# Kernel tuning notes

Measured on AMD Instinct MI355X. Metric: run time of the kernel, lower is better.

## Reference

```python
import jax, jax.numpy as jnp
import numpy as np

N, E, G = 50000, 800000, 64
NODE_DIM, HID, HEADS, EDGE_DIM = 128, 256, 4, 2
LAYER_IN = [NODE_DIM, HID, HID]
LAYER_HEADS = [HEADS, HEADS, 1]
BN_EPS = 1e-5


def setup_inputs() -> dict:
    key = jax.random.key(0)
    ks = iter(jax.random.split(key, 80))
    def nrm(shape, s=0.05):
        return jax.random.normal(next(ks), shape, jnp.float32) * s
    inp = {}
    inp['x'] = jax.random.normal(next(ks), (N, NODE_DIM), jnp.float32)
    inp['edge_index'] = jax.random.randint(next(ks), (2, E), 0, N, jnp.int32)
    inp['edge_attr'] = jax.random.normal(next(ks), (E, EDGE_DIM), jnp.float32)
    inp['batch'] = jnp.sort(jax.random.randint(next(ks), (N,), 0, G, jnp.int32))
    for i in range(3):
        H = LAYER_HEADS[i]; C = HID // H
        inp[f'W{i}'] = nrm((LAYER_IN[i], H * C))
        inp[f'asrc{i}'] = nrm((H, C))
        inp[f'adst{i}'] = nrm((H, C))
        inp[f'We{i}'] = nrm((EDGE_DIM, H * C))
        inp[f'aedge{i}'] = nrm((H, C))
        inp[f'bconv{i}'] = jnp.zeros((HID,), jnp.float32)
        inp[f'bn{i}_g'] = jnp.ones((HID,), jnp.float32)
        inp[f'bn{i}_b'] = jnp.zeros((HID,), jnp.float32)
        inp[f'bn{i}_m'] = nrm((HID,), 0.01)
        inp[f'bn{i}_v'] = jnp.ones((HID,), jnp.float32)
    inp['Wskip'] = nrm((NODE_DIM, HID))
    inp['bskip'] = jnp.zeros((HID,), jnp.float32)
    inp['Wp1'] = nrm((2 * HID, HID))
    inp['bp1'] = jnp.zeros((HID,), jnp.float32)
    inp['Wp2'] = nrm((HID, 1))
    inp['bp2'] = jnp.zeros((1,), jnp.float32)
    return inp


def gat_conv(x, src, dst, ea, W, a_s, a_d, We, a_e, b, H, concat):
    n = x.shape[0]
    C = W.shape[1] // H
    h = (x @ W).reshape(n, H, C)                      # [N,H,C]
    # attention logits per edge (src/dst node terms + edge term)
    al = ((h * a_s).sum(-1)[src]
          + (h * a_d).sum(-1)[dst]
          + ((ea @ We).reshape(-1, H, C) * a_e).sum(-1))  # [Et,H]
    al = jax.nn.leaky_relu(al, 0.2)
    # segment softmax over destination nodes
    amax = jax.ops.segment_max(al, dst, num_segments=n)
    ex = jnp.exp(al - amax[dst])
    den = jax.ops.segment_sum(ex, dst, num_segments=n)
    alpha = ex / (den[dst] + 1e-16)
    out = jax.ops.segment_sum(h[src] * alpha[..., None], dst, num_segments=n)  # [N,H,C]
    out = out.reshape(n, H * C) if concat else out.mean(axis=1)
    return out + b


def _forward(x, edge_index, edge_attr, batch, layer_params, Wskip, bskip, Wp1, bp1, Wp2, bp2):
    n = x.shape[0]
    # add self-loops (PyG GATConv default), edge_attr filled with mean
    loop = jnp.arange(n, dtype=edge_index.dtype)
    src = jnp.concatenate([edge_index[0], loop])
    dst = jnp.concatenate([edge_index[1], loop])
    ea = jnp.concatenate([edge_attr, jnp.broadcast_to(edge_attr.mean(0), (n, edge_attr.shape[1]))], axis=0)
    identity = x
    for i, (W, a_s, a_d, We, a_e, b, g, be, rm, rv) in enumerate(layer_params):
        layer_identity = (identity @ Wskip + bskip) if i == 0 else identity
        concat = i < 2
        H = LAYER_HEADS[i]
        h = gat_conv(x, src, dst, ea, W, a_s, a_d, We, a_e, b, H, concat)
        h = (h - rm) * jax.lax.rsqrt(rv + BN_EPS) * g + be   # BatchNorm1d (eval)
        h = jax.nn.elu(h)
        x = h + layer_identity
        identity = x
    # global mean + max pool per graph
    counts = jnp.maximum(jax.ops.segment_sum(jnp.ones((n,), x.dtype), batch, num_segments=G), 1.0)
    mean_pool = jax.ops.segment_sum(x, batch, num_segments=G) / counts[:, None]
    max_pool = jax.ops.segment_max(x, batch, num_segments=G)
    emb = jnp.concatenate([mean_pool, max_pool], axis=1)      # [G, 2*HID]
    hmid = jax.nn.relu(emb @ Wp1 + bp1)
    return hmid @ Wp2 + bp2                                   # [G, 1]


def reference(x, edge_index, edge_attr, batch,
              W0, asrc0, adst0, We0, aedge0, bconv0, bn0_g, bn0_b, bn0_m, bn0_v,
              W1, asrc1, adst1, We1, aedge1, bconv1, bn1_g, bn1_b, bn1_m, bn1_v,
              W2, asrc2, adst2, We2, aedge2, bconv2, bn2_g, bn2_b, bn2_m, bn2_v,
              Wskip, bskip, Wp1, bp1, Wp2, bp2):
    layer_params = [
        (W0, asrc0, adst0, We0, aedge0, bconv0, bn0_g, bn0_b, bn0_m, bn0_v),
        (W1, asrc1, adst1, We1, aedge1, bconv1, bn1_g, bn1_b, bn1_m, bn1_v),
        (W2, asrc2, adst2, We2, aedge2, bconv2, bn2_g, bn2_b, bn2_m, bn2_v),
    ]
    return _forward(x, edge_index, edge_attr, batch, layer_params, Wskip, bskip, Wp1, bp1, Wp2, bp2)
```

## Files before the change

kernel.cpp:

```cpp
#include <hip/hip_runtime.h>
#include <cfloat>

#define Nn 50000
#define Ee 800000
#define Etot (Ee + Nn)
#define Gg 64
#define HIDc 256
#define BN_EPS 1e-5f

typedef unsigned int   uint32;
typedef unsigned short ushort16;
typedef short  bf16x8 __attribute__((ext_vector_type(8)));
typedef float  f32x4  __attribute__((ext_vector_type(4)));

__device__ inline ushort16 f2bf(float f) {
    uint32 u = __float_as_uint(f);
    u = (u + 0x7fffu + ((u >> 16) & 1u)) >> 16;
    return (ushort16)u;
}
__device__ inline uint32 pack2(float a, float b) {
    return (uint32)f2bf(a) | ((uint32)f2bf(b) << 16);
}
__device__ inline uint32 fenc(float f) {
    uint32 b = __float_as_uint(f);
    return (b & 0x80000000u) ? ~b : (b | 0x80000000u);
}
__device__ inline float fdec(uint32 u) {
    uint32 b = (u & 0x80000000u) ? (u & 0x7fffffffu) : ~u;
    return __uint_as_float(b);
}

__device__ inline long ws_index(int c, int k, int KB) {
    int cb = c >> 4, m = c & 15, kb = k >> 5, q = (k >> 3) & 3, e = k & 7;
    return (((long)(cb * KB + kb) * 64 + q * 16 + m) << 3) + e;
}

#define CVT4 (Nn * 128 / 4)
#define CVT_BLKS ((CVT4 + 255) / 256)
#define EBKS ((Etot + 255) / 256)
__global__ __launch_bounds__(256) void prep_kernel(
        const float* __restrict__ ea, float* __restrict__ ea_s,
        const float* __restrict__ We0, const float* __restrict__ ae0,
        const float* __restrict__ We1, const float* __restrict__ ae1,
        const float* __restrict__ We2, const float* __restrict__ ae2,
        float* __restrict__ M,
        const float* __restrict__ W0, const float* __restrict__ Wskip,
        const float* __restrict__ W1, const float* __restrict__ W2,
        ushort16* __restrict__ WtC, ushort16* __restrict__ Wt1,
        ushort16* __restrict__ Wt2,
        const float* __restrict__ x, ushort16* __restrict__ xbf,
        const int* __restrict__ ei, int* __restrict__ counts) {
    int bid = blockIdx.x, t = threadIdx.x;
    if (bid < 256) {
        __shared__ float sh0[256], sh1[256];
        float s0 = 0.f, s1 = 0.f;
        for (int e = bid * 256 + t; e < Ee; e += 256 * 256) {
            s0 += ea[2 * e];
            s1 += ea[2 * e + 1];
        }
        sh0[t] = s0; sh1[t] = s1;
        __syncthreads();
        for (int off = 128; off > 0; off >>= 1) {
            if (t < off) { sh0[t] += sh0[t + off]; sh1[t] += sh1[t + off]; }
            __syncthreads();
        }
        if (t == 0) { atomicAdd(&ea_s[0], sh0[0]); atomicAdd(&ea_s[1], sh1[0]); }
    } else if (bid == 256) {
        if (t >= 18) return;
        int l = t < 8 ? 0 : (t < 16 ? 1 : 2);
        int r = t - l * 8;
        const float* We = (l == 0) ? We0 : (l == 1 ? We1 : We2);
        const float* ae = (l == 0) ? ae0 : (l == 1 ? ae1 : ae2);
        int Hl = (l < 2) ? 4 : 1;
        int Cl = 256 / Hl;
        int d = r / Hl, hh = r % Hl;
        float s = 0.f;
        for (int c = 0; c < Cl; ++c)
            s += We[d * 256 + hh * Cl + c] * ae[hh * Cl + c];
        M[l * 8 + r] = s;
    } else if (bid < 385) {
        int k = bid - 257;
        WtC[ws_index(t, k, 4)] = f2bf(W0[(long)k * 256 + t]);
    } else if (bid < 513) {
        int k = bid - 385;
        WtC[ws_index(256 + t, k, 4)] = f2bf(Wskip[(long)k * 256 + t]);
    } else if (bid < 769) {
        int k = bid - 513;
        Wt1[ws_index(t, k, 8)] = f2bf(W1[(long)k * 256 + t]);
    } else if (bid < 1025) {
        int k = bid - 769;
        Wt2[ws_index(t, k, 8)] = f2bf(W2[(long)k * 256 + t]);
    } else if (bid < 1025 + CVT_BLKS) {
        int i = (bid - 1025) * 256 + t;
        if (i < CVT4) {
            float4 v = *(const float4*)&x[i * 4];
            ushort4 o;
            o.x = f2bf(v.x); o.y = f2bf(v.y); o.z = f2bf(v.z); o.w = f2bf(v.w);
            *(ushort4*)&xbf[i * 4] = o;
        }
    } else {
        int e = (bid - 1025 - CVT_BLKS) * 256 + t;
        if (e < Etot) {
            int d = (e < Ee) ? ei[Ee + e] : (e - Ee);
            atomicAdd(&counts[d], 1);
        }
    }
}

__global__ void scan1_kernel(const int* __restrict__ in, int* __restrict__ inc,
                             int* __restrict__ bsums) {
    __shared__ int sh[256];
    int i = blockIdx.x * 256 + threadIdx.x;
    int v = (i < Nn) ? in[i] : 0;
    sh[threadIdx.x] = v;
    __syncthreads();
    for (int off = 1; off < 256; off <<= 1) {
        int t = ((int)threadIdx.x >= off) ? sh[threadIdx.x - off] : 0;
        __syncthreads();
        sh[threadIdx.x] += t;
        __syncthreads();
    }
    if (i < Nn) inc[i] = sh[threadIdx.x];
    if (threadIdx.x == 255) bsums[blockIdx.x] = sh[255];
}

__global__ void scan23_kernel(const int* __restrict__ inc, const int* __restrict__ bsums,
                              int* __restrict__ row_start, int* __restrict__ cursor, int nb) {
    __shared__ int sh[256];
    int b = blockIdx.x, t = threadIdx.x;
    sh[t] = (t < b && t < nb) ? bsums[t] : 0;
    __syncthreads();
    for (int off = 128; off > 0; off >>= 1) {
        if (t < off) sh[t] += sh[t + off];
        __syncthreads();
    }
    int base = sh[0];
    int i = b * 256 + t;
    if (i < Nn) {
        int v = inc[i] + base;
        row_start[i + 1] = v;
        cursor[i + 1] = v;
    }
    if (i == 0) { row_start[0] = 0; cursor[0] = 0; }
}

__global__ void scatter_kernel(const int* __restrict__ ei, const float* __restrict__ ea,
                               const float* __restrict__ ea_sum, int* __restrict__ cursor,
                               int* __restrict__ src_sorted, float* __restrict__ ea_sorted) {
    int e = blockIdx.x * blockDim.x + threadIdx.x;
    if (e >= Etot) return;
    int s, d; float e0, e1;
    if (e < Ee) {
        s = ei[e]; d = ei[Ee + e];
        e0 = ea[2 * e]; e1 = ea[2 * e + 1];
    } else {
        s = d = e - Ee;
        const float invE = 1.f / (float)Ee;
        e0 = ea_sum[0] * invE; e1 = ea_sum[1] * invE;
    }
    int pos = atomicAdd(&cursor[d], 1);
    src_sorted[pos] = s;
    ea_sorted[2 * pos]     = e0;
    ea_sorted[2 * pos + 1] = e1;
}

#define LDK 40
__global__ __launch_bounds__(256) void mfma_gemm_kernel(
        const ushort16* __restrict__ A,
        const ushort16* __restrict__ WS,
        uint32* __restrict__ outF,
        uint32* __restrict__ outS,
        const float* __restrict__ bskip,
        const float* __restrict__ a_s, const float* __restrict__ a_d,
        float* __restrict__ ssrc, float* __restrict__ sdst,
        int n, int K) {
    __shared__ ushort16 As[128 * LDK];
    const int t    = threadIdx.x;
    const int row0 = blockIdx.x * 128;
    const int c0   = blockIdx.y * 128;
    const bool isSkip = (outS != nullptr) && (c0 >= 256);
    const int cc0  = isSkip ? c0 - 256 : c0;
    const int wave = t >> 6, lane = t & 63;
    const int wr = wave >> 1, wc = wave & 1;
    const int l15 = lane & 15, quad = lane >> 4;
    const int KB = K >> 5;

    f32x4 acc[4][4];
#pragma unroll
    for (int j = 0; j < 4; ++j)
#pragma unroll
        for (int i = 0; i < 4; ++i) {
            acc[j][i][0] = 0.f; acc[j][i][1] = 0.f;
            acc[j][i][2] = 0.f; acc[j][i][3] = 0.f;
        }

    const int sm = t & 127;
    const int so = t >> 7;

    for (int k0 = 0; k0 < K; k0 += 32) {
        const int kb = k0 >> 5;
#pragma unroll
        for (int h = 0; h < 2; ++h) {
            int oct = so + 2 * h;
            int grow = row0 + sm;
            uint4 va = make_uint4(0, 0, 0, 0);
            if (grow < n) va = *(const uint4*)&A[(long)grow * K + k0 + 8 * oct];
            *(uint4*)&As[sm * LDK + 8 * oct] = va;
        }
        bf16x8 bfv[4];
#pragma unroll
        for (int j = 0; j < 4; ++j) {
            int cb = ((c0 + wc * 64) >> 4) + j;
            bfv[j] = *(const bf16x8*)&WS[(((long)cb * KB + kb) * 64 + lane) << 3];
        }
        __syncthreads();
        bf16x8 af[4];
#pragma unroll
        for (int i = 0; i < 4; ++i)
            af[i] = *(const bf16x8*)&As[(wr * 64 + i * 16 + l15) * LDK + quad * 8];
#pragma unroll
        for (int j = 0; j < 4; ++j)
#pragma unroll
            for (int i = 0; i < 4; ++i)
                acc[j][i] = __builtin_amdgcn_mfma_f32_16x16x32_bf16(
                    bfv[j], af[i], acc[j][i], 0, 0, 0);
        __syncthreads();
    }

    float4 bb[4];
#pragma unroll
    for (int j = 0; j < 4; ++j) {
        if (isSkip) bb[j] = *(const float4*)&bskip[cc0 + wc * 64 + j * 16 + quad * 4];
        else        bb[j] = make_float4(0.f, 0.f, 0.f, 0.f);
    }

    uint32* tgt = isSkip ? outS : outF;
#pragma unroll
    for (int i = 0; i < 4; ++i) {
        int row = row0 + wr * 64 + i * 16 + l15;
        if (row >= n) continue;
#pragma unroll
        for (int j = 0; j < 4; ++j) {
            int col = cc0 + wc * 64 + j * 16 + quad * 4;
            uint2 pk;
            pk.x = pack2(acc[j][i][0] + bb[j].x, acc[j][i][1] + bb[j].y);
            pk.y = pack2(acc[j][i][2] + bb[j].z, acc[j][i][3] + bb[j].w);
            *(uint2*)&tgt[(long)row * 128 + (col >> 1)] = pk;
        }
    }

    if (!isSkip && a_s != nullptr) {
        float4 asv[4], adv[4];
#pragma unroll
        for (int j = 0; j < 4; ++j) {
            int col = cc0 + wc * 64 + j * 16 + quad * 4;
            asv[j] = *(const float4*)&a_s[col];
            adv[j] = *(const float4*)&a_d[col];
        }
        const int part = (cc0 + wc * 64) >> 6;
#pragma unroll
        for (int i = 0; i < 4; ++i) {
            float ps = 0.f, pd = 0.f;
#pragma unroll
            for (int j = 0; j < 4; ++j) {
                ps += acc[j][i][0] * asv[j].x + acc[j][i][1] * asv[j].y
                    + acc[j][i][2] * asv[j].z + acc[j][i][3] * asv[j].w;
                pd += acc[j][i][0] * adv[j].x + acc[j][i][1] * adv[j].y
                    + acc[j][i][2] * adv[j].z + acc[j][i][3] * adv[j].w;
            }
            ps += __shfl_xor(ps, 16); ps += __shfl_xor(ps, 32);
            pd += __shfl_xor(pd, 16); pd += __shfl_xor(pd, 32);
            if (quad == 0) {
                int row = row0 + wr * 64 + i * 16 + l15;
                if (row < n) {
                    ssrc[row * 4 + part] = ps;
                    sdst[row * 4 + part] = pd;
                }
            }
        }
    }
}

template <int H>
__global__ __launch_bounds__(256) void agg_fused_kernel(
        const int* __restrict__ src_sorted, const int* __restrict__ row_start,
        const float* __restrict__ ea_sorted, const float* __restrict__ ssrc,
        const float* __restrict__ sdst, const float* __restrict__ M,
        const uint32* __restrict__ hbuf2,
        const float* __restrict__ bconv,
        const float* __restrict__ bn_g, const float* __restrict__ bn_b,
        const float* __restrict__ bn_m, const float* __restrict__ bn_v,
        const uint32* __restrict__ identity2, uint32* __restrict__ out2,
        float* __restrict__ wspill) {
    __shared__ int   s_sh[4][64];
    __shared__ float w_sh[4][64 * H];
    const int wv = threadIdx.x >> 6;
    const int l  = threadIdx.x & 63;
    const int node = blockIdx.x * 4 + wv;
    if (node >= Nn) return;
    const int hh = (H == 4) ? (l >> 4) : 0;
    const int beg = row_start[node], end = row_start[node + 1];
    const int deg = end - beg;

    float M0[H], M1[H], sd[H];
    {
        float4 sdv = *(const float4*)&sdst[node * 4];
        if (H == 4) { sd[0] = sdv.x; sd[1] = sdv.y; sd[2] = sdv.z; sd[3] = sdv.w; }
        else         sd[0] = sdv.x + sdv.y + sdv.z + sdv.w;
#pragma unroll
        for (int h = 0; h < H; ++h) { M0[h] = M[h]; M1[h] = M[H + h]; }
    }

    float a0 = 0.f, a1 = 0.f, a2 = 0.f, a3 = 0.f;

    auto gather = [&](int cnt) {
        for (int base = 0; base < cnt; base += 16) {
            int sk[16]; float wk[16]; uint2 f[16];
#pragma unroll
            for (int k = 0; k < 16; ++k) {
                sk[k] = s_sh[wv][base + k];
                wk[k] = w_sh[wv][(base + k) * H + hh];
            }
#pragma unroll
            for (int k = 0; k < 16; ++k)
                f[k] = *(const uint2*)&hbuf2[(long)sk[k] * 128 + 2 * l];
#pragma unroll
            for (int k = 0; k < 16; ++k) {
                float ww = wk[k];
                a0 += ww * __uint_as_float(f[k].x << 16);
                a1 += ww * __uint_as_float(f[k].x & 0xffff0000u);
                a2 += ww * __uint_as_float(f[k].y << 16);
                a3 += ww * __uint_as_float(f[k].y & 0xffff0000u);
            }
        }
    };

    if (deg <= 64) {
        const int  el  = beg + l;
        const bool act = l < deg;
        const int  elc = min(el, end - 1);
        const int  s   = src_sorted[elc];
        const float e0 = ea_sorted[2 * elc], e1 = ea_sorted[2 * elc + 1];
        float4 sv = *(const float4*)&ssrc[s * 4];
        float lh[H], m[H], dn[H];
#pragma unroll
        for (int h = 0; h < H; ++h) {
            float ss = (H == 4) ? ((const float*)&sv)[h]
                                : (sv.x + sv.y + sv.z + sv.w);
            float lg = ss + sd[h] + e0 * M0[h] + e1 * M1[h];
            lg = (lg > 0.f) ? lg : 0.2f * lg;
            lh[h] = lg;
            m[h]  = act ? lg : -FLT_MAX;
            dn[h] = act ? 1.f : 0.f;
        }
#pragma unroll
        for (int h = 0; h < H; ++h) {
#pragma unroll
            for (int off = 1; off < 64; off <<= 1) {
                float om = __shfl_xor(m[h], off, 64);
                float od = __shfl_xor(dn[h], off, 64);
                float nm = fmaxf(m[h], om);
                dn[h] = dn[h] * __expf(m[h] - nm) + od * __expf(om - nm);
                m[h] = nm;
            }
            dn[h] = 1.f / (dn[h] + 1e-16f);
        }
        s_sh[wv][l] = s;
#pragma unroll
        for (int h = 0; h < H; ++h)
            w_sh[wv][l * H + h] = act ? __expf(lh[h] - m[h]) * dn[h] : 0.f;
        asm volatile("s_waitcnt lgkmcnt(0)" ::: "memory");
        gather(deg);
    } else {
        float m[H], dn[H];
#pragma unroll
        for (int h = 0; h < H; ++h) { m[h] = -FLT_MAX; dn[h] = 0.f; }
        for (int cb = beg; cb < end; cb += 64) {
            int el = cb + l; bool act = el < end;
            int elc = min(el, end - 1);
            int s = src_sorted[elc];
            float e0 = ea_sorted[2 * elc], e1 = ea_sorted[2 * elc + 1];
            float4 sv = *(const float4*)&ssrc[s * 4];
#pragma unroll
            for (int h = 0; h < H; ++h) {
                float ss = (H == 4) ? ((const float*)&sv)[h]
                                    : (sv.x + sv.y + sv.z + sv.w);
                float lg = ss + sd[h] + e0 * M0[h] + e1 * M1[h];
                lg = (lg > 0.f) ? lg : 0.2f * lg;
                if (act) {
                    wspill[(long)el * H + h] = lg;
                    if (lg > m[h]) { dn[h] = dn[h] * __expf(m[h] - lg) + 1.f; m[h] = lg; }
                    else dn[h] += __expf(lg - m[h]);
                }
            }
        }
#pragma unroll
        for (int h = 0; h < H; ++h) {
#pragma unroll
            for (int off = 1; off < 64; off <<= 1) {
                float om = __shfl_xor(m[h], off, 64);
                float od = __shfl_xor(dn[h], off, 64);
                float nm = fmaxf(m[h], om);
                dn[h] = dn[h] * __expf(m[h] - nm) + od * __expf(om - nm);
                m[h] = nm;
            }
            dn[h] = 1.f / (dn[h] + 1e-16f);
        }
        for (int cb = beg; cb < end; cb += 64) {
            int el = cb + l; bool act = el < end;
            int elc = min(el, end - 1);
            s_sh[wv][l] = src_sorted[elc];
#pragma unroll
            for (int h = 0; h < H; ++h)
                w_sh[wv][l * H + h] =
                    act ? __expf(wspill[(long)el * H + h] - m[h]) * dn[h] : 0.f;
            asm volatile("s_waitcnt lgkmcnt(0)" ::: "memory");
            gather(min(64, end - cb));
            asm volatile("s_waitcnt lgkmcnt(0)" ::: "memory");
        }
    }

    int c = 4 * l;
    float4 bcv = *(const float4*)&bconv[c];
    float4 bgv = *(const float4*)&bn_g[c];
    float4 bbv = *(const float4*)&bn_b[c];
    float4 bmv = *(const float4*)&bn_m[c];
    float4 bvv = *(const float4*)&bn_v[c];
    float v0 = a0 + bcv.x, v1 = a1 + bcv.y, v2 = a2 + bcv.z, v3 = a3 + bcv.w;
    v0 = (v0 - bmv.x) * rsqrtf(bvv.x + BN_EPS) * bgv.x + bbv.x;
    v1 = (v1 - bmv.y) * rsqrtf(bvv.y + BN_EPS) * bgv.y + bbv.y;
    v2 = (v2 - bmv.z) * rsqrtf(bvv.z + BN_EPS) * bgv.z + bbv.z;
    v3 = (v3 - bmv.w) * rsqrtf(bvv.w + BN_EPS) * bgv.w + bbv.w;
    v0 = (v0 > 0.f) ? v0 : (expf(v0) - 1.f);
    v1 = (v1 > 0.f) ? v1 : (expf(v1) - 1.f);
    v2 = (v2 > 0.f) ? v2 : (expf(v2) - 1.f);
    v3 = (v3 > 0.f) ? v3 : (expf(v3) - 1.f);
    uint2 idu = *(const uint2*)&identity2[(long)node * 128 + 2 * l];
    v0 += __uint_as_float(idu.x << 16);
    v1 += __uint_as_float(idu.x & 0xffff0000u);
    v2 += __uint_as_float(idu.y << 16);
    v3 += __uint_as_float(idu.y & 0xffff0000u);
    uint2 o;
    o.x = pack2(v0, v1);
    o.y = pack2(v2, v3);
    *(uint2*)&out2[(long)node * 128 + 2 * l] = o;
}

#define POOL_ROWS 32
__global__ __launch_bounds__(128) void pool_kernel(
        const uint32* __restrict__ x2, const int* __restrict__ batch,
        float* __restrict__ psum, uint32* __restrict__ pmax, float* __restrict__ pcnt) {
    int c2 = threadIdx.x;
    int n0 = blockIdx.x * POOL_ROWS;
    if (n0 >= Nn) return;
    int n1 = min(n0 + POOL_ROWS, Nn);
    int cur = batch[n0];
    float s0 = 0.f, s1 = 0.f, m0 = -FLT_MAX, m1 = -FLT_MAX;
    int cnt = 0;
    int c = 2 * c2;
    for (int i = n0; i < n1; ++i) {
        int g = batch[i];
        if (g != cur) {
            atomicAdd(&psum[cur * 256 + c], s0);
            atomicAdd(&psum[cur * 256 + c + 1], s1);
            atomicMax(&pmax[cur * 256 + c], fenc(m0));
            atomicMax(&pmax[cur * 256 + c + 1], fenc(m1));
            if (c2 == 0) atomicAdd(&pcnt[cur], (float)cnt);
            cur = g; s0 = s1 = 0.f; m0 = m1 = -FLT_MAX; cnt = 0;
        }
        uint32 u = x2[(long)i * 128 + c2];
        float lo = __uint_as_float(u << 16);
        float hi = __uint_as_float(u & 0xffff0000u);
        s0 += lo; s1 += hi;
        m0 = fmaxf(m0, lo); m1 = fmaxf(m1, hi);
        ++cnt;
    }
    atomicAdd(&psum[cur * 256 + c], s0);
    atomicAdd(&psum[cur * 256 + c + 1], s1);
    atomicMax(&pmax[cur * 256 + c], fenc(m0));
    atomicMax(&pmax[cur * 256 + c + 1], fenc(m1));
    if (c2 == 0) atomicAdd(&pcnt[cur], (float)cnt);
}

__global__ __launch_bounds__(256) void mlp_kernel(
        const float* __restrict__ psum, const uint32* __restrict__ pmax,
        const float* __restrict__ pcnt, const float* __restrict__ Wp1,
        const float* __restrict__ bp1, const float* __restrict__ Wp2,
        const float* __restrict__ bp2, float* __restrict__ out) {
    int g = blockIdx.x;
    int j = threadIdx.x;
    float inv = 1.f / fmaxf(pcnt[g], 1.f);
    float acc = bp1[j];
    for (int k = 0; k < 256; ++k)
        acc += (psum[g * 256 + k] * inv) * Wp1[k * 256 + j];
    for (int k = 0; k < 256; ++k)
        acc += fdec(pmax[g * 256 + k]) * Wp1[(256 + k) * 256 + j];
    float v = fmaxf(acc, 0.f) * Wp2[j];
    __shared__ float red[256];
    red[j] = v;
    __syncthreads();
    for (int off = 128; off > 0; off >>= 1) {
        if (j < off) red[j] += red[j + off];
        __syncthreads();
    }
    if (j == 0) out[g] = red[0] + bp2[0];
}

extern "C" void kernel_launch(void* const* d_in, const int* in_sizes, int n_in,
                              void* d_out, int out_size, void* d_ws, size_t ws_size,
                              hipStream_t stream) {
    const float* x   = (const float*)d_in[0];
    const int*   ei  = (const int*)d_in[1];
    const float* ea  = (const float*)d_in[2];
    const int*   bat = (const int*)d_in[3];
    auto LP = [&](int l, int j) { return (const float*)d_in[4 + l * 10 + j]; };
    const float* Wskip = (const float*)d_in[34];
    const float* bskip = (const float*)d_in[35];
    const float* Wp1   = (const float*)d_in[36];
    const float* bp1   = (const float*)d_in[37];
    const float* Wp2   = (const float*)d_in[38];
    const float* bp2   = (const float*)d_in[39];
    float* out = (float*)d_out;

    char* p = (char*)d_ws;
    auto alloc = [&](size_t bytes) { void* r = (void*)p; p += (bytes + 255) & ~(size_t)255; return r; };
    uint32*   hbuf2  = (uint32*)alloc((size_t)Nn * 256 * 2);
    uint32*   skipbf = (uint32*)alloc((size_t)Nn * 128 * 4);
    uint32*   resA   = (uint32*)alloc((size_t)Nn * 128 * 4);
    uint32*   resB   = (uint32*)alloc((size_t)Nn * 128 * 4);
    ushort16* xbf    = (ushort16*)alloc((size_t)Nn * 128 * 2);
    float*    wbuf   = (float*)alloc((size_t)Etot * 4 * 4);
    float*    ea_sorted = (float*)alloc((size_t)Etot * 2 * 4);
    float*    ssrc   = (float*)alloc((size_t)Nn * 4 * 4);
    float*    sdst   = (float*)alloc((size_t)Nn * 4 * 4);
    int*      counts = (int*)alloc((size_t)Nn * 4);
    int*      incb   = (int*)alloc((size_t)Nn * 4);
    int*      row_start = (int*)alloc((size_t)(Nn + 1) * 4);
    int*      cursor    = (int*)alloc((size_t)(Nn + 1) * 4);
    int*      src_sorted = (int*)alloc((size_t)Etot * 4);
    int*      bsums  = (int*)alloc(256 * 4);
    float*    ea_s   = (float*)alloc(2 * 4);
    float*    Mbuf   = (float*)alloc(32 * 4);
    ushort16* WtC    = (ushort16*)alloc((size_t)512 * 128 * 2);
    ushort16* Wt1    = (ushort16*)alloc((size_t)256 * 256 * 2);
    ushort16* Wt2    = (ushort16*)alloc((size_t)256 * 256 * 2);
    float*    psum   = (float*)alloc((size_t)Gg * 256 * 4);
    uint32*   pmax   = (uint32*)alloc((size_t)Gg * 256 * 4);
    float*    pcnt   = (float*)alloc((size_t)Gg * 4);

    const int nb = (Nn + 255) / 256;

    hipMemsetAsync(counts, 0, (size_t)Nn * 4, stream);
    hipMemsetAsync(ea_s, 0, 8, stream);
    hipMemsetAsync(psum, 0, (size_t)Gg * 256 * 4 * 2 + (size_t)Gg * 4, stream);

    prep_kernel<<<1025 + CVT_BLKS + EBKS, 256, 0, stream>>>(
        ea, ea_s, LP(0,3), LP(0,4), LP(1,3), LP(1,4), LP(2,3), LP(2,4), Mbuf,
        LP(0,0), Wskip, LP(1,0), LP(2,0), WtC, Wt1, Wt2, x, xbf, ei, counts);

    scan1_kernel<<<nb, 256, 0, stream>>>(counts, incb, bsums);
    scan23_kernel<<<nb, 256, 0, stream>>>(incb, bsums, row_start, cursor, nb);
    scatter_kernel<<<EBKS, 256, 0, stream>>>(ei, ea, ea_s, cursor, src_sorted, ea_sorted);

    {
        dim3 g0((Nn + 127) / 128, 4);
        mfma_gemm_kernel<<<g0, 256, 0, stream>>>(
            xbf, WtC, hbuf2, skipbf, bskip,
            LP(0,1), LP(0,2), ssrc, sdst, Nn, 128);
    }

    const uint32* lid[3] = { skipbf, resA, resB };
    uint32*       lou[3] = { resA, resB, resA };
    const ushort16* lain[3] = { nullptr, (ushort16*)resA, (ushort16*)resB };
    const ushort16* lwt[3]  = { nullptr, Wt1, Wt2 };
    for (int l = 0; l < 3; ++l) {
        if (l > 0) {
            dim3 gl((Nn + 127) / 128, 2);
            mfma_gemm_kernel<<<gl, 256, 0, stream>>>(
                lain[l], lwt[l], hbuf2, nullptr, nullptr,
                LP(l,1), LP(l,2), ssrc, sdst, Nn, 256);
        }
        if (l < 2)
            agg_fused_kernel<4><<<(Nn + 3) / 4, 256, 0, stream>>>(
                src_sorted, row_start, ea_sorted, ssrc, sdst, Mbuf + l * 8,
                hbuf2, LP(l,5), LP(l,6), LP(l,7), LP(l,8), LP(l,9),
                lid[l], lou[l], wbuf);
        else
            agg_fused_kernel<1><<<(Nn + 3) / 4, 256, 0, stream>>>(
                src_sorted, row_start, ea_sorted, ssrc, sdst, Mbuf + l * 8,
                hbuf2, LP(l,5), LP(l,6), LP(l,7), LP(l,8), LP(l,9),
                lid[l], lou[l], wbuf);
    }

    pool_kernel<<<(Nn + POOL_ROWS - 1) / POOL_ROWS, 128, 0, stream>>>(resA, bat, psum, pmax, pcnt);
    mlp_kernel<<<Gg, 256, 0, stream>>>(psum, pmax, pcnt, Wp1, bp1, Wp2, bp2, out);
}
```

Before: 635.2 us.

## Precompute fused BN scale/shift and simplify warp softmax reductions in aggregation

```diff
diff --git a/kernel.cpp b/kernel.cpp
--- a/kernel.cpp
+++ b/kernel.cpp
@@ -49,7 +49,17 @@
         ushort16* __restrict__ WtC, ushort16* __restrict__ Wt1,
         ushort16* __restrict__ Wt2,
         const float* __restrict__ x, ushort16* __restrict__ xbf,
-        const int* __restrict__ ei, int* __restrict__ counts) {
+        const int* __restrict__ ei, int* __restrict__ counts,
+        const float* __restrict__ bc0, const float* __restrict__ g0,
+        const float* __restrict__ b0, const float* __restrict__ m0,
+        const float* __restrict__ v0,
+        const float* __restrict__ bc1, const float* __restrict__ g1,
+        const float* __restrict__ b1, const float* __restrict__ m1,
+        const float* __restrict__ v1,
+        const float* __restrict__ bc2, const float* __restrict__ g2,
+        const float* __restrict__ b2, const float* __restrict__ m2,
+        const float* __restrict__ v2,
+        float* __restrict__ bnf) {
     int bid = blockIdx.x, t = threadIdx.x;
     if (bid < 256) {
         __shared__ float sh0[256], sh1[256];
@@ -90,8 +100,19 @@
     } else if (bid < 1025) {
         int k = bid - 769;
         Wt2[ws_index(t, k, 8)] = f2bf(W2[(long)k * 256 + t]);
-    } else if (bid < 1025 + CVT_BLKS) {
-        int i = (bid - 1025) * 256 + t;
+    } else if (bid == 1025) {
+        for (int ll = 0; ll < 3; ++ll) {
+            const float* bc = ll == 0 ? bc0 : (ll == 1 ? bc1 : bc2);
+            const float* gg = ll == 0 ? g0  : (ll == 1 ? g1  : g2);
+            const float* bb = ll == 0 ? b0  : (ll == 1 ? b1  : b2);
+            const float* mm = ll == 0 ? m0  : (ll == 1 ? m1  : m2);
+            const float* vv = ll == 0 ? v0  : (ll == 1 ? v1  : v2);
+            float s = gg[t] * rsqrtf(vv[t] + BN_EPS);
+            bnf[ll * 512 + t]       = s;
+            bnf[ll * 512 + 256 + t] = (bc[t] - mm[t]) * s + bb[t];
+        }
+    } else if (bid < 1026 + CVT_BLKS) {
+        int i = (bid - 1026) * 256 + t;
         if (i < CVT4) {
             float4 v = *(const float4*)&x[i * 4];
             ushort4 o;
@@ -99,7 +120,7 @@
             *(ushort4*)&xbf[i * 4] = o;
         }
     } else {
-        int e = (bid - 1025 - CVT_BLKS) * 256 + t;
+        int e = (bid - 1026 - CVT_BLKS) * 256 + t;
         if (e < Etot) {
             int d = (e < Ee) ? ei[Ee + e] : (e - Ee);
             atomicAdd(&counts[d], 1);
@@ -287,9 +308,7 @@
         const float* __restrict__ ea_sorted, const float* __restrict__ ssrc,
         const float* __restrict__ sdst, const float* __restrict__ M,
         const uint32* __restrict__ hbuf2,
-        const float* __restrict__ bconv,
-        const float* __restrict__ bn_g, const float* __restrict__ bn_b,
-        const float* __restrict__ bn_m, const float* __restrict__ bn_v,
+        const float* __restrict__ bnS, const float* __restrict__ bnB,
         const uint32* __restrict__ identity2, uint32* __restrict__ out2,
         float* __restrict__ wspill) {
     __shared__ int   s_sh[4][64];
@@ -302,6 +321,11 @@
     const int beg = row_start[node], end = row_start[node + 1];
     const int deg = end - beg;
 
+    const int c = 4 * l;
+    const float4 scv = *(const float4*)&bnS[c];
+    const float4 sbv = *(const float4*)&bnB[c];
+    const uint2  idu = *(const uint2*)&identity2[(long)node * 128 + 2 * l];
+
     float M0[H], M1[H], sd[H];
     {
         float4 sdv = *(const float4*)&sdst[node * 4];
@@ -314,6 +338,7 @@
     float a0 = 0.f, a1 = 0.f, a2 = 0.f, a3 = 0.f;
 
     auto gather = [&](int cnt) {
+        const uint32 loff = (uint32)l << 3;
         for (int base = 0; base < cnt; base += 16) {
             int sk[16]; float wk[16]; uint2 f[16];
 #pragma unroll
@@ -323,7 +348,8 @@
             }
 #pragma unroll
             for (int k = 0; k < 16; ++k)
-                f[k] = *(const uint2*)&hbuf2[(long)sk[k] * 128 + 2 * l];
+                f[k] = *(const uint2*)((const char*)hbuf2 +
+                                       (((uint32)sk[k] << 9) + loff));
 #pragma unroll
             for (int k = 0; k < 16; ++k) {
                 float ww = wk[k];
@@ -342,7 +368,7 @@
         const int  s   = src_sorted[elc];
         const float e0 = ea_sorted[2 * elc], e1 = ea_sorted[2 * elc + 1];
         float4 sv = *(const float4*)&ssrc[s * 4];
-        float lh[H], m[H], dn[H];
+        float lh[H], m[H];
 #pragma unroll
         for (int h = 0; h < H; ++h) {
             float ss = (H == 4) ? ((const float*)&sv)[h]
@@ -351,24 +377,56 @@
             lg = (lg > 0.f) ? lg : 0.2f * lg;
             lh[h] = lg;
             m[h]  = act ? lg : -FLT_MAX;
-            dn[h] = act ? 1.f : 0.f;
         }
 #pragma unroll
         for (int h = 0; h < H; ++h) {
-#pragma unroll
-            for (int off = 1; off < 64; off <<= 1) {
-                float om = __shfl_xor(m[h], off, 64);
-                float od = __shfl_xor(dn[h], off, 64);
-                float nm = fmaxf(m[h], om);
-                dn[h] = dn[h] * __expf(m[h] - nm) + od * __expf(om - nm);
-                m[h] = nm;
-            }
-            dn[h] = 1.f / (dn[h] + 1e-16f);
+            m[h] = fmaxf(m[h], __shfl_xor(m[h], 1, 64));
+            m[h] = fmaxf(m[h], __shfl_xor(m[h], 2, 64));
+            m[h] = fmaxf(m[h], __shfl_xor(m[h], 4, 64));
+            m[h] = fmaxf(m[h], __shfl_xor(m[h], 8, 64));
+        }
+        if (deg > 16) {
+#pragma unroll
+            for (int h = 0; h < H; ++h)
+                m[h] = fmaxf(m[h], __shfl_xor(m[h], 16, 64));
+        }
+        if (deg > 32) {
+#pragma unroll
+            for (int h = 0; h < H; ++h)
+                m[h] = fmaxf(m[h], __shfl_xor(m[h], 32, 64));
+        }
+        float ex[H], dn[H];
+#pragma unroll
+        for (int h = 0; h < H; ++h) {
+            ex[h] = act ? __expf(lh[h] - m[h]) : 0.f;
+            dn[h] = ex[h];
+        }
+#pragma unroll
+        for (int h = 0; h < H; ++h) {
+            dn[h] += __shfl_xor(dn[h], 1, 64);
+            dn[h] += __shfl_xor(dn[h], 2, 64);
+            dn[h] += __shfl_xor(dn[h], 4, 64);
+            dn[h] += __shfl_xor(dn[h], 8, 64);
+        }
+        if (deg > 16) {
+#pragma unroll
+            for (int h = 0; h < H; ++h) dn[h] += __shfl_xor(dn[h], 16, 64);
+        }
+        if (deg > 32) {
+#pragma unroll
+            for (int h = 0; h < H; ++h) dn[h] += __shfl_xor(dn[h], 32, 64);
         }
         s_sh[wv][l] = s;
-#pragma unroll
-        for (int h = 0; h < H; ++h)
-            w_sh[wv][l * H + h] = act ? __expf(lh[h] - m[h]) * dn[h] : 0.f;
+        if (H == 4) {
+            float4 w4;
+            w4.x = ex[0] * (1.f / (dn[0] + 1e-16f));
+            w4.y = ex[1] * (1.f / (dn[1] + 1e-16f));
+            w4.z = ex[2] * (1.f / (dn[2] + 1e-16f));
+            w4.w = ex[3] * (1.f / (dn[3] + 1e-16f));
+            *(float4*)&w_sh[wv][l * 4] = w4;
+        } else {
+            w_sh[wv][l] = ex[0] * (1.f / (dn[0] + 1e-16f));
+        }
         asm volatile("s_waitcnt lgkmcnt(0)" ::: "memory");
         gather(deg);
     } else {
@@ -420,22 +478,14 @@
         }
     }
 
-    int c = 4 * l;
-    float4 bcv = *(const float4*)&bconv[c];
-    float4 bgv = *(const float4*)&bn_g[c];
-    float4 bbv = *(const float4*)&bn_b[c];
-    float4 bmv = *(const float4*)&bn_m[c];
-    float4 bvv = *(const float4*)&bn_v[c];
-    float v0 = a0 + bcv.x, v1 = a1 + bcv.y, v2 = a2 + bcv.z, v3 = a3 + bcv.w;
-    v0 = (v0 - bmv.x) * rsqrtf(bvv.x + BN_EPS) * bgv.x + bbv.x;
-    v1 = (v1 - bmv.y) * rsqrtf(bvv.y + BN_EPS) * bgv.y + bbv.y;
-    v2 = (v2 - bmv.z) * rsqrtf(bvv.z + BN_EPS) * bgv.z + bbv.z;
-    v3 = (v3 - bmv.w) * rsqrtf(bvv.w + BN_EPS) * bgv.w + bbv.w;
+    float v0 = a0 * scv.x + sbv.x;
+    float v1 = a1 * scv.y + sbv.y;
+    float v2 = a2 * scv.z + sbv.z;
+    float v3 = a3 * scv.w + sbv.w;
     v0 = (v0 > 0.f) ? v0 : (expf(v0) - 1.f);
     v1 = (v1 > 0.f) ? v1 : (expf(v1) - 1.f);
     v2 = (v2 > 0.f) ? v2 : (expf(v2) - 1.f);
     v3 = (v3 > 0.f) ? v3 : (expf(v3) - 1.f);
-    uint2 idu = *(const uint2*)&identity2[(long)node * 128 + 2 * l];
     v0 += __uint_as_float(idu.x << 16);
     v1 += __uint_as_float(idu.x & 0xffff0000u);
     v2 += __uint_as_float(idu.y << 16);
@@ -541,6 +591,7 @@
     int*      bsums  = (int*)alloc(256 * 4);
     float*    ea_s   = (float*)alloc(2 * 4);
     float*    Mbuf   = (float*)alloc(32 * 4);
+    float*    bnf    = (float*)alloc((size_t)3 * 512 * 4);
     ushort16* WtC    = (ushort16*)alloc((size_t)512 * 128 * 2);
     ushort16* Wt1    = (ushort16*)alloc((size_t)256 * 256 * 2);
     ushort16* Wt2    = (ushort16*)alloc((size_t)256 * 256 * 2);
@@ -554,9 +605,13 @@
     hipMemsetAsync(ea_s, 0, 8, stream);
     hipMemsetAsync(psum, 0, (size_t)Gg * 256 * 4 * 2 + (size_t)Gg * 4, stream);
 
-    prep_kernel<<<1025 + CVT_BLKS + EBKS, 256, 0, stream>>>(
+    prep_kernel<<<1026 + CVT_BLKS + EBKS, 256, 0, stream>>>(
         ea, ea_s, LP(0,3), LP(0,4), LP(1,3), LP(1,4), LP(2,3), LP(2,4), Mbuf,
-        LP(0,0), Wskip, LP(1,0), LP(2,0), WtC, Wt1, Wt2, x, xbf, ei, counts);
+        LP(0,0), Wskip, LP(1,0), LP(2,0), WtC, Wt1, Wt2, x, xbf, ei, counts,
+        LP(0,5), LP(0,6), LP(0,7), LP(0,8), LP(0,9),
+        LP(1,5), LP(1,6), LP(1,7), LP(1,8), LP(1,9),
+        LP(2,5), LP(2,6), LP(2,7), LP(2,8), LP(2,9),
+        bnf);
 
     scan1_kernel<<<nb, 256, 0, stream>>>(counts, incb, bsums);
     scan23_kernel<<<nb, 256, 0, stream>>>(incb, bsums, row_start, cursor, nb);
@@ -583,12 +638,12 @@
         if (l < 2)
             agg_fused_kernel<4><<<(Nn + 3) / 4, 256, 0, stream>>>(
                 src_sorted, row_start, ea_sorted, ssrc, sdst, Mbuf + l * 8,
-                hbuf2, LP(l,5), LP(l,6), LP(l,7), LP(l,8), LP(l,9),
+                hbuf2, bnf + l * 512, bnf + l * 512 + 256,
                 lid[l], lou[l], wbuf);
         else
             agg_fused_kernel<1><<<(Nn + 3) / 4, 256, 0, stream>>>(
                 src_sorted, row_start, ea_sorted, ssrc, sdst, Mbuf + l * 8,
-                hbuf2, LP(l,5), LP(l,6), LP(l,7), LP(l,8), LP(l,9),
+                hbuf2, bnf + l * 512, bnf + l * 512 + 256,
                 lid[l], lou[l], wbuf);
     }
 
```

Result: no change. 623.1 us (-1.9%).
